# Optimization experiments

Measured on AMD Instinct MI355X. Metric: run time of the kernel, lower is better.

Reference implementation:

```python
import jax, jax.numpy as jnp
import numpy as np

EPS = 1e-6

def _l2norm_axis1(x):
    # torch Normalize(2): divide by L2 norm over dim 1 (the T axis of [B,T,F])
    return x / jnp.sqrt(jnp.sum(x * x, axis=1, keepdims=True))

def _mlp(x, w1, b1, w2, b2):
    # frame_MLPEmbed / freq_MLPEmbed share structure: linear-relu-linear-l2norm(dim=1)
    h = jax.nn.relu(x @ w1 + b1)
    return _l2norm_axis1(h @ w2 + b2)

def _reshape_feat(f):
    # [L,B,C,T,D] -> permute(0,2,1,3) per layer -> [L,B,T,C*D]
    L, B, C, T, D = f.shape
    return jnp.transpose(f, (0, 1, 3, 2, 4)).reshape(L, B, T, C * D)

def _cos_time(x):
    # x: [L,B,T,C]; cosine sims between frames within each batch item -> [L,B,T,T]
    xn = x / (jnp.sqrt(jnp.sum(x * x, axis=-1, keepdims=True)) + EPS)
    S = (jnp.einsum('lbtc,lbsc->lbts', xn, xn) + 1.0) * 0.5
    return S / jnp.sum(S, axis=-1, keepdims=True)

def _cos_freq(x):
    # cosine sims between batch items per frame, returned as [L,B,T,B]
    xn = x / (jnp.sqrt(jnp.sum(x * x, axis=-1, keepdims=True)) + EPS)
    S = (jnp.einsum('lbtc,latc->lbta', xn, xn) + 1.0) * 0.5
    return S / jnp.sum(S, axis=-1, keepdims=True)

def _forward(feat_s, feat_t, tk_w1, tk_b1, tk_w2, tk_b2, fk_w1, fk_b1, fk_w2, fk_b2,
             tq_w1, tq_b1, tq_w2, tq_b2, fq_w1, fq_b1, fq_w2, fq_b2):
    feat_t = jax.lax.stop_gradient(feat_t)  # detach=True
    xs = _reshape_feat(feat_s)  # [s_len,B,T,CD]
    xt = _reshape_feat(feat_t)  # [t_len,B,T,CD]
    s_len, t_len = xs.shape[0], xt.shape[0]

    # gram matrices used for key/query MLPs
    sim_t = jnp.einsum('lbtc,lbsc->lbts', xt, xt)    # [t_len,B,T,T]
    sim_t_g = jnp.einsum('lbtc,latc->lbta', xt, xt)  # [t_len,B,T,B]
    sim_s = jnp.einsum('lbtc,lbsc->lbts', xs, xs)    # [s_len,B,T,T]
    sim_s_g = jnp.einsum('lbtc,latc->lbta', xs, xs)  # [s_len,B,T,B]

    mlp_v = jax.vmap(_mlp)  # vmap over the per-layer MLPs
    tk = mlp_v(sim_t, tk_w1, tk_b1, tk_w2, tk_b2)     # [t_len,B,T,T]
    fk = mlp_v(sim_t_g, fk_w1, fk_b1, fk_w2, fk_b2)   # [t_len,B,T,32]
    tq = mlp_v(sim_s, tq_w1, tq_b1, tq_w2, tq_b2)     # [s_len,B,T,T]
    fq = mlp_v(sim_s_g, fq_w1, fq_b1, fq_w2, fq_b2)   # [s_len,B,T,32]

    time_key = jnp.moveaxis(tk, 0, -1)    # [B,T,T,t_len]
    freq_key = jnp.moveaxis(fk, 0, -1)    # [B,T,32,t_len]
    time_query = jnp.moveaxis(tq, 0, 2)   # [B,T,s_len,T]
    freq_query = jnp.moveaxis(fq, 0, 2)   # [B,T,s_len,32]

    time_att = jax.nn.softmax(jnp.matmul(time_query, time_key), axis=-1)  # [B,T,s_len,t_len]
    freq_att = jax.nn.softmax(jnp.matmul(freq_query, freq_key), axis=-1)  # [B,T,s_len,t_len]

    stu_time = _cos_time(xs)  # [s_len,B,T,T]
    tea_time = _cos_time(xt)  # [t_len,B,T,T]
    stu_freq = _cos_freq(xs)  # [s_len,B,T,B]
    tea_freq = _cos_freq(xt)  # [t_len,B,T,B]

    # the torch nested lists are [i][j]; student entries depend only on i, teacher only on j
    stu_time_b = jnp.broadcast_to(stu_time[:, None], (s_len, t_len) + stu_time.shape[1:])
    stu_freq_b = jnp.broadcast_to(stu_freq[:, None], (s_len, t_len) + stu_freq.shape[1:])
    tea_time_b = jnp.broadcast_to(tea_time[None, :], (s_len, t_len) + tea_time.shape[1:])
    tea_freq_b = jnp.broadcast_to(tea_freq[None, :], (s_len, t_len) + tea_freq.shape[1:])

    return (stu_time_b, stu_freq_b, tea_time_b, tea_freq_b, time_att, freq_att)

def setup_inputs() -> dict:
    key = jax.random.key(0)
    ks = jax.random.split(key, 20)
    s_len, t_len, B, C, T, D = 4, 4, 8, 64, 256, 16
    H = 2 * T  # frame MLP hidden
    F = 32     # bsz * factor
    p = lambda k, shp: jax.random.normal(k, shp, dtype=jnp.float32) * 0.02
    return {
        'feat_s': jax.random.normal(ks[0], (s_len, B, C, T, D), dtype=jnp.float32),
        'feat_t': jax.random.normal(ks[1], (t_len, B, C, T, D), dtype=jnp.float32),
        'tk_w1': p(ks[2], (t_len, T, H)), 'tk_b1': p(ks[3], (t_len, H)),
        'tk_w2': p(ks[4], (t_len, H, T)), 'tk_b2': p(ks[5], (t_len, T)),
        'fk_w1': p(ks[6], (t_len, B, F)), 'fk_b1': p(ks[7], (t_len, F)),
        'fk_w2': p(ks[8], (t_len, F, F)), 'fk_b2': p(ks[9], (t_len, F)),
        'tq_w1': p(ks[10], (s_len, T, H)), 'tq_b1': p(ks[11], (s_len, H)),
        'tq_w2': p(ks[12], (s_len, H, T)), 'tq_b2': p(ks[13], (s_len, T)),
        'fq_w1': p(ks[14], (s_len, B, F)), 'fq_b1': p(ks[15], (s_len, F)),
        'fq_w2': p(ks[16], (s_len, F, F)), 'fq_b2': p(ks[17], (s_len, F)),
    }

def reference(feat_s, feat_t, tk_w1, tk_b1, tk_w2, tk_b2, fk_w1, fk_b1, fk_w2, fk_b2,
              tq_w1, tq_b1, tq_w2, tq_b2, fq_w1, fq_b1, fq_w2, fq_b2):
    return _forward(feat_s, feat_t, tk_w1, tk_b1, tk_w2, tk_b2, fk_w1, fk_b1, fk_w2, fk_b2,
                    tq_w1, tq_b1, tq_w2, tq_b2, fq_w1, fq_b1, fq_w2, fq_b2)
```

## Files before the change

kernel.cpp:

```cpp
#include <hip/hip_runtime.h>
#include <math.h>

typedef _Float16 half_t;
typedef _Float16 h2 __attribute__((ext_vector_type(2)));
typedef _Float16 h4 __attribute__((ext_vector_type(4)));
typedef _Float16 h8 __attribute__((ext_vector_type(8)));
typedef float f4 __attribute__((ext_vector_type(4)));
static constexpr float REPS = 1e-6f;

__global__ __launch_bounds__(256) void k_prep2(const float* __restrict__ tkw1, const float* __restrict__ tqw1,
                                               const float* __restrict__ tkw2, const float* __restrict__ tqw2,
                                               const float* __restrict__ tkb1, const float* __restrict__ tqb1,
                                               const float* __restrict__ tkb2, const float* __restrict__ tqb2,
                                               half_t* __restrict__ W1t, half_t* __restrict__ W2t,
                                               float* __restrict__ Bc1, float* __restrict__ Bc2,
                                               float* __restrict__ part,
                                               const float* __restrict__ fs, const float* __restrict__ ft,
                                               half_t* __restrict__ Xh, float* __restrict__ nrm) {
  __shared__ float T[64][65];
  int bid = blockIdx.x;
  int tid = threadIdx.x;
  if (bid < 256) {
    int z = bid >> 5, tile = bid & 31;
    int kt = tile >> 3, ntile = tile & 7;
    const float* src = (z < 4 ? tkw1 : tqw1) + (size_t)(z & 3) * 256 * 512;
#pragma unroll
    for (int q = 0; q < 16; q++) {
      int e = q * 256 + tid;
      int r = e >> 6, c = e & 63;
      T[r][c] = src[(size_t)(kt * 64 + r) * 512 + ntile * 64 + c];
    }
    __syncthreads();
#pragma unroll
    for (int q = 0; q < 16; q++) {
      int e = q * 256 + tid;
      int nn = e >> 6, kk = e & 63;
      W1t[(size_t)z * 512 * 256 + (size_t)(ntile * 64 + nn) * 256 + kt * 64 + kk] = (half_t)T[kk][nn];
    }
  } else if (bid < 512) {
    int bb = bid - 256;
    int z = bb >> 5, tile = bb & 31;
    int kt = tile >> 2, ntile = tile & 3;
    const float* src = (z < 4 ? tkw2 : tqw2) + (size_t)(z & 3) * 512 * 256;
#pragma unroll
    for (int q = 0; q < 16; q++) {
      int e = q * 256 + tid;
      int r = e >> 6, c = e & 63;
      T[r][c] = src[(size_t)(kt * 64 + r) * 256 + ntile * 64 + c];
    }
    __syncthreads();
#pragma unroll
    for (int q = 0; q < 16; q++) {
      int e = q * 256 + tid;
      int nn = e >> 6, kk = e & 63;
      W2t[(size_t)z * 256 * 512 + (size_t)(ntile * 64 + nn) * 512 + kt * 64 + kk] = (half_t)T[kk][nn];
    }
  } else if (bid == 512) {
    for (int e = tid; e < 4096; e += 256) {
      int z = e >> 9, n = e & 511;
      Bc1[e] = (z < 4 ? tkb1 : tqb1)[(z & 3) * 512 + n];
    }
    for (int e = tid; e < 2048; e += 256) {
      int z = e >> 8, n = e & 255;
      Bc2[e] = (z < 4 ? tkb2 : tqb2)[(z & 3) * 256 + n];
    }
    for (int e = tid; e < 16384; e += 256) part[e] = 0.f;
  } else {
    int bid2 = bid - 513;
    int tensor = bid2 >> 7;
    int l = (bid2 >> 5) & 3;
    int b = (bid2 >> 2) & 7;
    int tc = bid2 & 3;
    int tl = tid >> 2;
    int d0 = (tid & 3) * 4;
    int t = tc * 64 + tl;
    const float* base = (tensor ? ft : fs) + (size_t)((l * 8 + b) * 64) * 4096 + t * 16 + d0;
    size_t row = (size_t)(tensor * 32 + l * 8 + b) * 256 + t;
    half_t* xrow = Xh + row * 1024 + d0;
    float acc = 0.f;
#pragma unroll 8
    for (int c = 0; c < 64; c++) {
      float4 v = *(const float4*)(base + (size_t)c * 4096);
      acc += v.x * v.x + v.y * v.y + v.z * v.z + v.w * v.w;
      h4 hv;
      hv[0] = (half_t)v.x; hv[1] = (half_t)v.y; hv[2] = (half_t)v.z; hv[3] = (half_t)v.w;
      *(h4*)(xrow + c * 16) = hv;
    }
    acc += __shfl_xor(acc, 1);
    acc += __shfl_xor(acc, 2);
    if ((tid & 3) == 0) nrm[row] = sqrtf(acc);
  }
}

__global__ __launch_bounds__(512) void k_gs(const half_t* __restrict__ Xh,
                                            const float* __restrict__ nrm,
                                            half_t* __restrict__ simh,
                                            float* __restrict__ out_stu,
                                            float* __restrict__ out_tea,
                                            float* __restrict__ simg) {
  __shared__ __align__(16) char smem[66048];
  int bid = blockIdx.x;
  int tid = threadIdx.x;
  if (bid < 256) {
    half_t* Bsm = (half_t*)smem;
    float* rspart = (float*)(smem + 32768);
    float* rowsumS = (float*)(smem + 32768 + 1024);
    int mt = bid & 3;
    int z = bid >> 2;
    const half_t* Bb = Xh + (size_t)z * 256 * 1024;
    int w = tid >> 6, lane = tid & 63;
    int wm = w >> 2, wn = w & 3;
    int lr = lane & 15, lg = lane >> 4;
    f4 acc[2][4] = {};
    int r0 = tid >> 3, seg0 = tid & 7;
    int sw0 = (seg0 ^ (r0 & 7)) * 8;
    for (int kc = 0; kc < 1024; kc += 64) {
      h8 bv[4];
#pragma unroll
      for (int it = 0; it < 4; it++)
        bv[it] = *(const h8*)(Bb + (size_t)(it * 64 + r0) * 1024 + kc + seg0 * 8);
      __syncthreads();
#pragma unroll
      for (int it = 0; it < 4; it++)
        *(h8*)(Bsm + (it * 64 + r0) * 64 + sw0) = bv[it];
      __syncthreads();
#pragma unroll
      for (int kk = 0; kk < 2; kk++) {
        int g = kk * 4 + lg;
        h8 af[2], bf[4];
#pragma unroll
        for (int mf = 0; mf < 2; mf++) {
          int rA = mt * 64 + wm * 32 + mf * 16 + lr;
          af[mf] = *(const h8*)(Bsm + rA * 64 + ((g ^ (rA & 7)) * 8));
        }
#pragma unroll
        for (int nf = 0; nf < 4; nf++) {
          int rB = wn * 64 + nf * 16 + lr;
          bf[nf] = *(const h8*)(Bsm + rB * 64 + ((g ^ (rB & 7)) * 8));
        }
#pragma unroll
        for (int mf = 0; mf < 2; mf++)
#pragma unroll
          for (int nf = 0; nf < 4; nf++)
            acc[mf][nf] = __builtin_amdgcn_mfma_f32_16x16x32_f16(af[mf], bf[nf], acc[mf][nf], 0, 0, 0);
      }
    }
    int tensor = z >> 5, l = (z >> 3) & 3, b = z & 7;
    const float* nz = nrm + z * 256;
    float nc[4];
    int cols[4];
#pragma unroll
    for (int nf = 0; nf < 4; nf++) {
      cols[nf] = wn * 64 + nf * 16 + lr;
      nc[nf] = nz[cols[nf]] + REPS;
    }
    float v[2][4][4];
    float rowpart[2][4];
#pragma unroll
    for (int mf = 0; mf < 2; mf++) {
#pragma unroll
      for (int rg = 0; rg < 4; rg++) {
        int rib = wm * 32 + mf * 16 + lg * 4 + rg;
        float nr = nz[mt * 64 + rib] + REPS;
        float p = 0.f;
#pragma unroll
        for (int nf = 0; nf < 4; nf++) {
          float S = acc[mf][nf][rg];
          float vv = fmaf(S / (nr * nc[nf]), 0.5f, 0.5f);
          v[mf][nf][rg] = vv;
          p += vv;
          simh[(size_t)z * 65536 + (size_t)(mt * 64 + rib) * 256 + cols[nf]] = (half_t)S;
        }
        rowpart[mf][rg] = p;
      }
    }
#pragma unroll
    for (int mf = 0; mf < 2; mf++)
#pragma unroll
      for (int rg = 0; rg < 4; rg++) {
        float p = rowpart[mf][rg];
        p += __shfl_xor(p, 1); p += __shfl_xor(p, 2);
        p += __shfl_xor(p, 4); p += __shfl_xor(p, 8);
        rowpart[mf][rg] = p;
      }
    if (lr == 0) {
#pragma unroll
      for (int mf = 0; mf < 2; mf++)
#pragma unroll
        for (int rg = 0; rg < 4; rg++)
          rspart[(wm * 32 + mf * 16 + lg * 4 + rg) * 4 + wn] = rowpart[mf][rg];
    }
    __syncthreads();
    if (tid < 64)
      rowsumS[tid] = rspart[tid * 4] + rspart[tid * 4 + 1] + rspart[tid * 4 + 2] + rspart[tid * 4 + 3];
    __syncthreads();
    float* outp = tensor ? out_tea : out_stu;
#pragma unroll
    for (int mf = 0; mf < 2; mf++) {
#pragma unroll
      for (int rg = 0; rg < 4; rg++) {
        int rib = wm * 32 + mf * 16 + lg * 4 + rg;
        int t = mt * 64 + rib;
        float inv = 1.f / rowsumS[rib];
#pragma unroll
        for (int nf = 0; nf < 4; nf++) {
          float val = v[mf][nf][rg] * inv;
          size_t inner = ((size_t)(b * 256 + t)) * 256 + cols[nf];
          if (tensor == 0) {
            size_t base = (size_t)l * 4 * 524288;
#pragma unroll
            for (int j = 0; j < 4; j++) outp[base + (size_t)j * 524288 + inner] = val;
          } else {
#pragma unroll
            for (int i = 0; i < 4; i++) outp[((size_t)(i * 4 + l)) * 524288 + inner] = val;
          }
        }
      }
    }
  } else {
    half_t* X = (half_t*)smem;
    int sb = bid - 256;
    int tensor = sb >> 8;
    int l = (sb >> 6) & 3;
    int tc = sb & 63;
    int t0 = tc * 4;
#pragma unroll
    for (int j = 0; j < 8; j++) {
      int i = j * 512 + tid;
      int r = i >> 7, col = i & 127;
      int b = r & 7, tl = r >> 3;
      const half_t* src = Xh + ((size_t)(tensor * 32 + l * 8 + b) * 256 + t0 + tl) * 1024 + col * 8;
      *(h8*)(X + r * 1032 + col * 8) = *(const h8*)src;
    }
    __syncthreads();
    if (tid < 256) {
      int tl = tid >> 6;
      int ab = tid & 63;
      int b = ab >> 3, a = ab & 7;
      const half_t* xa = X + (tl * 8 + b) * 1032;
      const half_t* xb = X + (tl * 8 + a) * 1032;
      float acc = 0.f;
#pragma unroll 8
      for (int k = 0; k < 1024; k += 8) {
        h8 va = *(const h8*)(xa + k);
        h8 vb = *(const h8*)(xb + k);
#if __has_builtin(__builtin_amdgcn_fdot2)
#pragma unroll
        for (int i = 0; i < 4; i++) {
          h2 pa, pb;
          pa[0] = va[2 * i]; pa[1] = va[2 * i + 1];
          pb[0] = vb[2 * i]; pb[1] = vb[2 * i + 1];
          acc = __builtin_amdgcn_fdot2(pa, pb, acc, false);
        }
#else
#pragma unroll
        for (int e = 0; e < 8; e++) acc += (float)va[e] * (float)vb[e];
#endif
      }
      simg[(size_t)tensor * 65536 + ((size_t)(l * 8 + b) * 256 + t0 + tl) * 8 + a] = acc;
    }
  }
}

__global__ __launch_bounds__(256) void k_m1s(const half_t* __restrict__ simh,
                                             const half_t* __restrict__ W1t,
                                             const float* __restrict__ Bc1,
                                             half_t* __restrict__ hbuf,
                                             const float* __restrict__ simg,
                                             const float* __restrict__ n,
                                             float* __restrict__ out_stu, float* __restrict__ out_tea,
                                             const float* __restrict__ qw1, const float* __restrict__ qb1,
                                             const float* __restrict__ qw2, const float* __restrict__ qb2,
                                             const float* __restrict__ kw1, const float* __restrict__ kb1,
                                             const float* __restrict__ kw2, const float* __restrict__ kb2,
                                             float* __restrict__ qout, float* __restrict__ kout) {
  __shared__ __align__(16) char smem[40352];
  int bid = blockIdx.x;
  int tid = threadIdx.x;
  if (bid < 512) {
    constexpr int K = 256, N = 512;
    half_t* Asm = (half_t*)smem;
    half_t* Bsm = (half_t*)(smem + 16384);
    int mt = bid & 15, nt = (bid >> 4) & 3, z = bid >> 6;
    int l = z & 3, path = z >> 2;
    const half_t* Ab = simh + ((size_t)((path == 0 ? 32 : 0) + l * 8)) * 256 * 256;
    const half_t* Bb = W1t + (size_t)z * 512 * 256;
    half_t* Ob = hbuf + (size_t)z * 2048 * 512;
    int wave = tid >> 6, lane = tid & 63;
    int wm = (wave >> 1) * 64, wn = (wave & 1) * 64;
    int lr = lane & 15, lg = lane >> 4;
    f4 acc[4][4] = {};
    int r0 = tid >> 3, seg0 = tid & 7;
    int sw0 = (seg0 ^ (r0 & 7)) * 8;
    for (int kc = 0; kc < K; kc += 64) {
      h8 av[4], bv[4];
#pragma unroll
      for (int j = 0; j < 4; j++) {
        av[j] = *(const h8*)(Ab + (size_t)(mt * 128 + r0 + 32 * j) * K + kc + seg0 * 8);
        bv[j] = *(const h8*)(Bb + (size_t)(nt * 128 + r0 + 32 * j) * K + kc + seg0 * 8);
      }
      __syncthreads();
#pragma unroll
      for (int j = 0; j < 4; j++) {
        *(h8*)(Asm + (r0 + 32 * j) * 64 + sw0) = av[j];
        *(h8*)(Bsm + (r0 + 32 * j) * 64 + sw0) = bv[j];
      }
      __syncthreads();
#pragma unroll
      for (int kk = 0; kk < 2; kk++) {
        h8 af[4], bf[4];
#pragma unroll
        for (int mf = 0; mf < 4; mf++) {
          int r = wm + mf * 16 + lr;
          af[mf] = *(const h8*)(Asm + r * 64 + (((kk * 4 + lg) ^ (r & 7)) * 8));
        }
#pragma unroll
        for (int nf = 0; nf < 4; nf++) {
          int r = wn + nf * 16 + lr;
          bf[nf] = *(const h8*)(Bsm + r * 64 + (((kk * 4 + lg) ^ (r & 7)) * 8));
        }
#pragma unroll
        for (int mf = 0; mf < 4; mf++)
#pragma unroll
          for (int nf = 0; nf < 4; nf++)
            acc[mf][nf] = __builtin_amdgcn_mfma_f32_16x16x32_f16(af[mf], bf[nf], acc[mf][nf], 0, 0, 0);
      }
    }
#pragma unroll
    for (int nf = 0; nf < 4; nf++) {
      int col = nt * 128 + wn + nf * 16 + lr;
      float bv2 = Bc1[z * N + col];
#pragma unroll
      for (int mf = 0; mf < 4; mf++) {
#pragma unroll
        for (int rg = 0; rg < 4; rg++) {
          int row = mt * 128 + wm + mf * 16 + lg * 4 + rg;
          float v = fmaxf(acc[mf][nf][rg] + bv2, 0.f);
          Ob[(size_t)row * N + col] = (half_t)v;
        }
      }
    }
  } else if (bid < 576) {
    int bb = bid - 512;
    int tensor = bb >> 5;
    int lb = bb & 31;
    const float* sg = simg + (size_t)tensor * 65536;
    const float* nb2 = n + tensor * 8192;
    float* out = tensor ? out_tea : out_stu;
    int l = lb >> 3, b = lb & 7;
    int a = tid & 7;
    for (int tc = 0; tc < 8; tc++) {
      int t = tc * 32 + (tid >> 3);
      float nb = nb2[lb * 256 + t] + REPS;
      float na = nb2[(l * 8 + a) * 256 + t] + REPS;
      float v = (sg[((size_t)lb * 256 + t) * 8 + a] / (nb * na) + 1.f) * 0.5f;
      float w = v;
      for (int m = 1; m < 8; m <<= 1) w += __shfl_xor(w, m);
      v /= w;
      size_t inner = ((size_t)(b * 256 + t)) * 8 + a;
      if (tensor == 0) {
#pragma unroll
        for (int j = 0; j < 4; j++) out[((size_t)(l * 4 + j)) * 16384 + inner] = v;
      } else {
#pragma unroll
        for (int i = 0; i < 4; i++) out[((size_t)(i * 4 + l)) * 16384 + inner] = v;
      }
    }
  } else {
    float* sw1 = (float*)smem;
    float* sb1 = (float*)(smem + 1024);
    float* sw2 = (float*)(smem + 1152);
    float* sb2 = (float*)(smem + 5248);
    float* zs  = (float*)(smem + 5376);
    float* pcn = (float*)(smem + 39168);
    float* cn  = (float*)(smem + 40224);
    int bb = bid - 576;
    int tensor = bb >> 5;
    int lb = bb & 31;
    int l = lb >> 3;
    const float* w1 = tensor ? kw1 : qw1;
    const float* b1 = tensor ? kb1 : qb1;
    const float* w2 = tensor ? kw2 : qw2;
    const float* b2 = tensor ? kb2 : qb2;
    const float* sg = simg + (size_t)tensor * 65536;
    float* outp = tensor ? kout : qout;
    int t = tid;
    sw1[t] = w1[l * 256 + t];
    if (t < 32) { sb1[t] = b1[l * 32 + t]; sb2[t] = b2[l * 32 + t]; }
    for (int q = t; q < 1024; q += 256) sw2[q] = w2[l * 1024 + q];
    __syncthreads();
    float x[8];
#pragma unroll
    for (int a = 0; a < 8; a++) x[a] = sg[((size_t)lb * 256 + t) * 8 + a];
    float h[32];
#pragma unroll
    for (int f = 0; f < 32; f++) {
      float acc = sb1[f];
#pragma unroll
      for (int a = 0; a < 8; a++) acc += x[a] * sw1[a * 32 + f];
      h[f] = fmaxf(acc, 0.f);
    }
#pragma unroll
    for (int g = 0; g < 32; g++) {
      float acc = sb2[g];
#pragma unroll
      for (int f = 0; f < 32; f++) acc += h[f] * sw2[f * 32 + g];
      zs[t * 33 + g] = acc;
    }
    __syncthreads();
    {
      int col = t & 31, ch = t >> 5;
      float sq = 0.f;
      for (int r = ch * 32; r < ch * 32 + 32; r++) { float v = zs[r * 33 + col]; sq += v * v; }
      pcn[ch * 33 + col] = sq;
    }
    __syncthreads();
    if (t < 32) {
      float ssum = 0.f;
#pragma unroll
      for (int c = 0; c < 8; c++) ssum += pcn[c * 33 + t];
      cn[t] = sqrtf(ssum);
    }
    __syncthreads();
#pragma unroll
    for (int g = 0; g < 32; g++)
      outp[((size_t)lb * 256 + t) * 32 + g] = zs[t * 33 + g] / cn[g];
  }
}

__global__ __launch_bounds__(256) void k_mfma2(const half_t* __restrict__ A,
                                               const half_t* __restrict__ Bt,
                                               const float* __restrict__ bias,
                                               half_t* __restrict__ out,
                                               float* __restrict__ part) {
  constexpr int K = 512, N = 256;
  __shared__ __align__(16) half_t Asm[128 * 64];
  __shared__ __align__(16) half_t Bsm[128 * 64];
  int z = blockIdx.z;
  const half_t* Ab = A + (size_t)z * 2048 * 512;
  const half_t* Bb = Bt + (size_t)z * 256 * 512;
  half_t* Ob = out + (size_t)z * 2048 * 256;
  int mt = blockIdx.x, nt = blockIdx.y;
  int tid = threadIdx.x;
  int wave = tid >> 6, lane = tid & 63;
  int wm = (wave >> 1) * 64, wn = (wave & 1) * 64;
  int lr = lane & 15, lg = lane >> 4;
  f4 acc[4][4] = {};
  int r0 = tid >> 3, seg0 = tid & 7;
  int sw0 = (seg0 ^ (r0 & 7)) * 8;
  for (int kc = 0; kc < K; kc += 64) {
    h8 av[4], bv[4];
#pragma unroll
    for (int j = 0; j < 4; j++) {
      av[j] = *(const h8*)(Ab + (size_t)(mt * 128 + r0 + 32 * j) * K + kc + seg0 * 8);
      bv[j] = *(const h8*)(Bb + (size_t)(nt * 128 + r0 + 32 * j) * K + kc + seg0 * 8);
    }
    __syncthreads();
#pragma unroll
    for (int j = 0; j < 4; j++) {
      *(h8*)(Asm + (r0 + 32 * j) * 64 + sw0) = av[j];
      *(h8*)(Bsm + (r0 + 32 * j) * 64 + sw0) = bv[j];
    }
    __syncthreads();
#pragma unroll
    for (int kk = 0; kk < 2; kk++) {
      h8 af[4], bf[4];
#pragma unroll
      for (int mf = 0; mf < 4; mf++) {
        int r = wm + mf * 16 + lr;
        af[mf] = *(const h8*)(Asm + r * 64 + (((kk * 4 + lg) ^ (r & 7)) * 8));
      }
#pragma unroll
      for (int nf = 0; nf < 4; nf++) {
        int r = wn + nf * 16 + lr;
        bf[nf] = *(const h8*)(Bsm + r * 64 + (((kk * 4 + lg) ^ (r & 7)) * 8));
      }
#pragma unroll
      for (int mf = 0; mf < 4; mf++)
#pragma unroll
        for (int nf = 0; nf < 4; nf++)
          acc[mf][nf] = __builtin_amdgcn_mfma_f32_16x16x32_f16(af[mf], bf[nf], acc[mf][nf], 0, 0, 0);
    }
  }
#pragma unroll
  for (int nf = 0; nf < 4; nf++) {
    int col = nt * 128 + wn + nf * 16 + lr;
    float bv2 = bias[z * N + col];
    float colsq = 0.f;
#pragma unroll
    for (int mf = 0; mf < 4; mf++) {
#pragma unroll
      for (int rg = 0; rg < 4; rg++) {
        int row = mt * 128 + wm + mf * 16 + lg * 4 + rg;
        float v = acc[mf][nf][rg] + bv2;
        Ob[(size_t)row * N + col] = (half_t)v;
        colsq += v * v;
      }
    }
    colsq += __shfl_xor(colsq, 16);
    colsq += __shfl_xor(colsq, 32);
    if (lg == 0) {
      int b = mt >> 1;
      atomicAdd(&part[((z * 8 + b) << 8) + col], colsq);
    }
  }
}

__global__ __launch_bounds__(64) void k_att(const half_t* __restrict__ Zq,
                                            const half_t* __restrict__ Zk,
                                            const float* __restrict__ part,
                                            const float* __restrict__ fq,
                                            const float* __restrict__ fk,
                                            float* __restrict__ out_time,
                                            float* __restrict__ out_freq) {
  int bid = blockIdx.x;
  int lane = threadIdx.x;
  if (bid < 2048) {
    int b = bid >> 8, t = bid & 255;
    float acc[4][4];
#pragma unroll
    for (int i = 0; i < 4; i++)
#pragma unroll
      for (int j = 0; j < 4; j++) acc[i][j] = 0.f;
    for (int it = 0; it < 4; it++) {
      int s = lane + it * 64;
      float qv[4], kv[4];
#pragma unroll
      for (int i = 0; i < 4; i++) {
        size_t lbO = (size_t)(i * 8 + b);
        float pq = part[(((4 + i) * 8 + b) << 8) + s];
        float pk = part[(((i) * 8 + b) << 8) + s];
        qv[i] = (float)Zq[(lbO * 256 + t) * 256 + s] * rsqrtf(pq);
        kv[i] = (float)Zk[(lbO * 256 + t) * 256 + s] * rsqrtf(pk);
      }
#pragma unroll
      for (int i = 0; i < 4; i++)
#pragma unroll
        for (int j = 0; j < 4; j++) acc[i][j] += qv[i] * kv[j];
    }
#pragma unroll
    for (int i = 0; i < 4; i++)
#pragma unroll
      for (int j = 0; j < 4; j++)
        for (int m = 32; m >= 1; m >>= 1) acc[i][j] += __shfl_xor(acc[i][j], m);
    if (lane < 16) {
      int i = lane >> 2, j = lane & 3;
      float mx = fmaxf(fmaxf(acc[i][0], acc[i][1]), fmaxf(acc[i][2], acc[i][3]));
      float sum = expf(acc[i][0] - mx) + expf(acc[i][1] - mx) + expf(acc[i][2] - mx) + expf(acc[i][3] - mx);
      out_time[(size_t)bid * 16 + lane] = expf(acc[i][j] - mx) / sum;
    }
  } else {
    int pair = bid - 2048;
    int b = pair >> 7, tp = pair & 127;
    int t = tp * 2 + (lane >> 5);
    int f = lane & 31;
    float qv[4], kv[4];
#pragma unroll
    for (int i = 0; i < 4; i++) {
      size_t lbO = (size_t)(i * 8 + b);
      qv[i] = fq[(lbO * 256 + t) * 32 + f];
      kv[i] = fk[(lbO * 256 + t) * 32 + f];
    }
    float acc[4][4];
#pragma unroll
    for (int i = 0; i < 4; i++)
#pragma unroll
      for (int j = 0; j < 4; j++) acc[i][j] = qv[i] * kv[j];
#pragma unroll
    for (int i = 0; i < 4; i++)
#pragma unroll
      for (int j = 0; j < 4; j++)
        for (int m = 16; m >= 1; m >>= 1) acc[i][j] += __shfl_xor(acc[i][j], m);
    int fl = lane & 31;
    if (fl < 16) {
      int i = fl >> 2, j = fl & 3;
      float mx = fmaxf(fmaxf(acc[i][0], acc[i][1]), fmaxf(acc[i][2], acc[i][3]));
      float sum = expf(acc[i][0] - mx) + expf(acc[i][1] - mx) + expf(acc[i][2] - mx) + expf(acc[i][3] - mx);
      out_freq[((size_t)(b * 256 + t)) * 16 + fl] = expf(acc[i][j] - mx) / sum;
    }
  }
}

extern "C" void kernel_launch(void* const* d_in, const int* in_sizes, int n_in,
                              void* d_out, int out_size, void* d_ws, size_t ws_size,
                              hipStream_t stream) {
  (void)in_sizes; (void)n_in; (void)out_size; (void)ws_size;
  const float* feat_s = (const float*)d_in[0];
  const float* feat_t = (const float*)d_in[1];
  const float* tk_w1 = (const float*)d_in[2];
  const float* tk_b1 = (const float*)d_in[3];
  const float* tk_w2 = (const float*)d_in[4];
  const float* tk_b2 = (const float*)d_in[5];
  const float* fk_w1 = (const float*)d_in[6];
  const float* fk_b1 = (const float*)d_in[7];
  const float* fk_w2 = (const float*)d_in[8];
  const float* fk_b2 = (const float*)d_in[9];
  const float* tq_w1 = (const float*)d_in[10];
  const float* tq_b1 = (const float*)d_in[11];
  const float* tq_w2 = (const float*)d_in[12];
  const float* tq_b2 = (const float*)d_in[13];
  const float* fq_w1 = (const float*)d_in[14];
  const float* fq_b1 = (const float*)d_in[15];
  const float* fq_w2 = (const float*)d_in[16];
  const float* fq_b2 = (const float*)d_in[17];

  float* ws = (float*)d_ws;
  half_t* Xh   = (half_t*)ws;
  half_t* hbuf = (half_t*)ws;
  half_t* Zbuf = (half_t*)(ws + 4194304);
  half_t* simh = (half_t*)(ws + 8388608);
  half_t* W1t  = (half_t*)(ws + 10485760);
  half_t* W2t  = (half_t*)(ws + 11010048);
  float* Bc1   = ws + 11534336;
  float* Bc2   = ws + 11538432;
  float* simg  = ws + 11540480;
  float* nrm   = ws + 11671552;
  float* part  = ws + 11687936;
  float* fkb   = ws + 11704320;
  float* fqb   = ws + 11966464;

  float* out = (float*)d_out;
  float* out_stu_time = out;
  float* out_stu_freq = out + 8388608;
  float* out_tea_time = out + 8650752;
  float* out_tea_freq = out + 17039360;
  float* out_time_att = out + 17301504;
  float* out_freq_att = out + 17334272;

  hipLaunchKernelGGL(k_prep2, dim3(769), dim3(256), 0, stream,
                     tk_w1, tq_w1, tk_w2, tq_w2, tk_b1, tq_b1, tk_b2, tq_b2,
                     W1t, W2t, Bc1, Bc2, part, feat_s, feat_t, Xh, nrm);
  hipLaunchKernelGGL(k_gs, dim3(768), dim3(512), 0, stream,
                     Xh, nrm, simh, out_stu_time, out_tea_time, simg);
  hipLaunchKernelGGL(k_m1s, dim3(640), dim3(256), 0, stream,
                     simh, W1t, Bc1, hbuf, simg, nrm,
                     out_stu_freq, out_tea_freq,
                     fq_w1, fq_b1, fq_w2, fq_b2, fk_w1, fk_b1, fk_w2, fk_b2, fqb, fkb);
  hipLaunchKernelGGL(k_mfma2, dim3(16, 2, 8), dim3(256), 0, stream,
                     hbuf, W2t, Bc2, Zbuf, part);
  hipLaunchKernelGGL(k_att, dim3(3072), dim3(64), 0, stream,
                     Zbuf + (size_t)4 * 2048 * 256, Zbuf, part, fqb, fkb,
                     out_time_att, out_freq_att);
}
```

Before: 124.2 us.

## Halve k_gs group-sim shared tile and restructure k_att into 256-thread blocks

The group-similarity branch of k_gs now stages the 1024-wide rows in two 512-wide halves, roughly halving its shared memory footprint. This should raise occupancy for the whole kernel, at the cost of an extra barrier pass. k_att is reworked from 3072 single-wave blocks into 384 four-wave blocks. Each block precomputes the inverse column norms into shared memory once, and each wave handles four time steps with vectorized 4-wide half loads instead of strided scalar loads. This cuts redundant rsqrt and part-array reads and improves load width, but gives fewer blocks and more serial work per wave.

```diff
diff --git a/kernel.cpp b/kernel.cpp
--- a/kernel.cpp
+++ b/kernel.cpp
@@ -98,7 +98,7 @@
                                             float* __restrict__ out_stu,
                                             float* __restrict__ out_tea,
                                             float* __restrict__ simg) {
-  __shared__ __align__(16) char smem[66048];
+  __shared__ __align__(16) char smem[34048];
   int bid = blockIdx.x;
   int tid = threadIdx.x;
   if (bid < 256) {
@@ -224,41 +224,46 @@
     int l = (sb >> 6) & 3;
     int tc = sb & 63;
     int t0 = tc * 4;
-#pragma unroll
-    for (int j = 0; j < 8; j++) {
-      int i = j * 512 + tid;
-      int r = i >> 7, col = i & 127;
-      int b = r & 7, tl = r >> 3;
-      const half_t* src = Xh + ((size_t)(tensor * 32 + l * 8 + b) * 256 + t0 + tl) * 1024 + col * 8;
-      *(h8*)(X + r * 1032 + col * 8) = *(const h8*)src;
-    }
-    __syncthreads();
-    if (tid < 256) {
-      int tl = tid >> 6;
-      int ab = tid & 63;
-      int b = ab >> 3, a = ab & 7;
-      const half_t* xa = X + (tl * 8 + b) * 1032;
-      const half_t* xb = X + (tl * 8 + a) * 1032;
-      float acc = 0.f;
+    float acc = 0.f;
+    int tl_c = tid >> 6;
+    int ab = tid & 63;
+    int bb = ab >> 3, aa = ab & 7;
+    for (int kh = 0; kh < 2; kh++) {
+#pragma unroll
+      for (int j = 0; j < 4; j++) {
+        int i = j * 512 + tid;
+        int r = i >> 6, col = i & 63;
+        int b = r & 7, tl = r >> 3;
+        const half_t* src = Xh + ((size_t)(tensor * 32 + l * 8 + b) * 256 + t0 + tl) * 1024
+                               + kh * 512 + col * 8;
+        *(h8*)(X + r * 520 + col * 8) = *(const h8*)src;
+      }
+      __syncthreads();
+      if (tid < 256) {
+        const half_t* xa = X + (tl_c * 8 + bb) * 520;
+        const half_t* xb = X + (tl_c * 8 + aa) * 520;
 #pragma unroll 8
-      for (int k = 0; k < 1024; k += 8) {
-        h8 va = *(const h8*)(xa + k);
-        h8 vb = *(const h8*)(xb + k);
+        for (int k = 0; k < 512; k += 8) {
+          h8 va = *(const h8*)(xa + k);
+          h8 vb = *(const h8*)(xb + k);
 #if __has_builtin(__builtin_amdgcn_fdot2)
 #pragma unroll
-        for (int i = 0; i < 4; i++) {
-          h2 pa, pb;
-          pa[0] = va[2 * i]; pa[1] = va[2 * i + 1];
-          pb[0] = vb[2 * i]; pb[1] = vb[2 * i + 1];
-          acc = __builtin_amdgcn_fdot2(pa, pb, acc, false);
-        }
+          for (int i = 0; i < 4; i++) {
+            h2 pa, pb;
+            pa[0] = va[2 * i]; pa[1] = va[2 * i + 1];
+            pb[0] = vb[2 * i]; pb[1] = vb[2 * i + 1];
+            acc = __builtin_amdgcn_fdot2(pa, pb, acc, false);
+          }
 #else
 #pragma unroll
-        for (int e = 0; e < 8; e++) acc += (float)va[e] * (float)vb[e];
+          for (int e = 0; e < 8; e++) acc += (float)va[e] * (float)vb[e];
 #endif
-      }
-      simg[(size_t)tensor * 65536 + ((size_t)(l * 8 + b) * 256 + t0 + tl) * 8 + a] = acc;
-    }
+        }
+      }
+      __syncthreads();
+    }
+    if (tid < 256)
+      simg[(size_t)tensor * 65536 + ((size_t)(l * 8 + bb) * 256 + t0 + tl_c) * 8 + aa] = acc;
   }
 }
 
@@ -506,51 +511,66 @@
   }
 }
 
-__global__ __launch_bounds__(64) void k_att(const half_t* __restrict__ Zq,
-                                            const half_t* __restrict__ Zk,
-                                            const float* __restrict__ part,
-                                            const float* __restrict__ fq,
-                                            const float* __restrict__ fk,
-                                            float* __restrict__ out_time,
-                                            float* __restrict__ out_freq) {
+__global__ __launch_bounds__(256) void k_att(const half_t* __restrict__ Zq,
+                                             const half_t* __restrict__ Zk,
+                                             const float* __restrict__ part,
+                                             const float* __restrict__ fq,
+                                             const float* __restrict__ fk,
+                                             float* __restrict__ out_time,
+                                             float* __restrict__ out_freq) {
+  __shared__ float invq[4][256], invk[4][256];
   int bid = blockIdx.x;
-  int lane = threadIdx.x;
-  if (bid < 2048) {
-    int b = bid >> 8, t = bid & 255;
-    float acc[4][4];
-#pragma unroll
-    for (int i = 0; i < 4; i++)
-#pragma unroll
-      for (int j = 0; j < 4; j++) acc[i][j] = 0.f;
-    for (int it = 0; it < 4; it++) {
-      int s = lane + it * 64;
-      float qv[4], kv[4];
+  int tid = threadIdx.x;
+  if (bid < 128) {
+    int b = bid >> 4, tc = bid & 15;
+    for (int e = tid; e < 1024; e += 256) {
+      int i = e >> 8, s = e & 255;
+      invq[i][s] = rsqrtf(part[(((4 + i) * 8 + b) << 8) + s]);
+      invk[i][s] = rsqrtf(part[((i * 8 + b) << 8) + s]);
+    }
+    __syncthreads();
+    int w = tid >> 6, lane = tid & 63;
+    int s0 = lane * 4;
+#pragma unroll
+    for (int tt = 0; tt < 4; tt++) {
+      int t = tc * 16 + w * 4 + tt;
+      float qv[4][4], kv[4][4];
 #pragma unroll
       for (int i = 0; i < 4; i++) {
         size_t lbO = (size_t)(i * 8 + b);
-        float pq = part[(((4 + i) * 8 + b) << 8) + s];
-        float pk = part[(((i) * 8 + b) << 8) + s];
-        qv[i] = (float)Zq[(lbO * 256 + t) * 256 + s] * rsqrtf(pq);
-        kv[i] = (float)Zk[(lbO * 256 + t) * 256 + s] * rsqrtf(pk);
-      }
+        h4 qh = *(const h4*)(Zq + (lbO * 256 + t) * 256 + s0);
+        h4 kh = *(const h4*)(Zk + (lbO * 256 + t) * 256 + s0);
+#pragma unroll
+        for (int e = 0; e < 4; e++) {
+          qv[i][e] = (float)qh[e] * invq[i][s0 + e];
+          kv[i][e] = (float)kh[e] * invk[i][s0 + e];
+        }
+      }
+      float acc[4][4];
 #pragma unroll
       for (int i = 0; i < 4; i++)
 #pragma unroll
-        for (int j = 0; j < 4; j++) acc[i][j] += qv[i] * kv[j];
-    }
-#pragma unroll
-    for (int i = 0; i < 4; i++)
-#pragma unroll
-      for (int j = 0; j < 4; j++)
-        for (int m = 32; m >= 1; m >>= 1) acc[i][j] += __shfl_xor(acc[i][j], m);
-    if (lane < 16) {
-      int i = lane >> 2, j = lane & 3;
-      float mx = fmaxf(fmaxf(acc[i][0], acc[i][1]), fmaxf(acc[i][2], acc[i][3]));
-      float sum = expf(acc[i][0] - mx) + expf(acc[i][1] - mx) + expf(acc[i][2] - mx) + expf(acc[i][3] - mx);
-      out_time[(size_t)bid * 16 + lane] = expf(acc[i][j] - mx) / sum;
+        for (int j = 0; j < 4; j++) {
+          float a = 0.f;
+#pragma unroll
+          for (int e = 0; e < 4; e++) a += qv[i][e] * kv[j][e];
+          acc[i][j] = a;
+        }
+#pragma unroll
+      for (int i = 0; i < 4; i++)
+#pragma unroll
+        for (int j = 0; j < 4; j++)
+          for (int m = 32; m >= 1; m >>= 1) acc[i][j] += __shfl_xor(acc[i][j], m);
+      if (lane < 16) {
+        int i = lane >> 2, j = lane & 3;
+        float mx = fmaxf(fmaxf(acc[i][0], acc[i][1]), fmaxf(acc[i][2], acc[i][3]));
+        float sum = expf(acc[i][0] - mx) + expf(acc[i][1] - mx) + expf(acc[i][2] - mx) + expf(acc[i][3] - mx);
+        out_time[((size_t)(b * 256 + t)) * 16 + lane] = expf(acc[i][j] - mx) / sum;
+      }
     }
   } else {
-    int pair = bid - 2048;
+    int sub = tid >> 6, lane = tid & 63;
+    int pair = (bid - 128) * 4 + sub;
     int b = pair >> 7, tp = pair & 127;
     int t = tp * 2 + (lane >> 5);
     int f = lane & 31;
@@ -638,7 +658,7 @@
                      fq_w1, fq_b1, fq_w2, fq_b2, fk_w1, fk_b1, fk_w2, fk_b2, fqb, fkb);
   hipLaunchKernelGGL(k_mfma2, dim3(16, 2, 8), dim3(256), 0, stream,
                      hbuf, W2t, Bc2, Zbuf, part);
-  hipLaunchKernelGGL(k_att, dim3(3072), dim3(64), 0, stream,
+  hipLaunchKernelGGL(k_att, dim3(384), dim3(256), 0, stream,
                      Zbuf + (size_t)4 * 2048 * 256, Zbuf, part, fqb, fkb,
                      out_time_att, out_freq_att);
 }
```

Result: faster. 111.9 us (-9.9%).
